# Performance work log

Hardware: AMD Instinct MI355X
Metric: run time of the kernel (lower is better)

## Reference

```python
import jax, jax.numpy as jnp
import numpy as np
import math

B, S, D = 16, 1, 4096
H, KVH, HD = 32, 8, 128
MAXB, MAXS = 16, 4096
R = H // KVH  # n_rep


def _rope(t, cos, sin):
    # t: [B, S, h, HD]; cos/sin: [S, HD//2]
    tf = t.astype(jnp.float32).reshape(*t.shape[:-1], HD // 2, 2)
    a, b = tf[..., 0], tf[..., 1]
    c = cos[None, :, None, :]
    s = sin[None, :, None, :]
    out = jnp.stack([a * c - b * s, a * s + b * c], axis=-1)
    return out.reshape(t.shape).astype(t.dtype)


def setup_inputs() -> dict:
    key = jax.random.key(0)
    ks = jax.random.split(key, 9)
    scale = 1.0 / math.sqrt(D)
    ang = jax.random.uniform(ks[7], (S, HD // 2), jnp.float32) * (2.0 * np.pi)
    return {
        "x": jax.random.normal(ks[0], (B, S, D), jnp.float32),
        "start_pos": 4095,
        "freqs_cos": jnp.cos(ang),
        "freqs_sin": jnp.sin(ang),
        "cache_k": jax.random.normal(ks[1], (MAXB, MAXS, KVH, HD), jnp.float32),
        "cache_v": jax.random.normal(ks[2], (MAXB, MAXS, KVH, HD), jnp.float32),
        "wq": jax.random.normal(ks[3], (D, H * HD), jnp.float32) * scale,
        "wk": jax.random.normal(ks[4], (D, KVH * HD), jnp.float32) * scale,
        "wv": jax.random.normal(ks[5], (D, KVH * HD), jnp.float32) * scale,
        "wo": jax.random.normal(ks[6], (H * HD, D), jnp.float32) * scale,
    }


def reference(x, start_pos, freqs_cos, freqs_sin, cache_k, cache_v, wq, wk, wv, wo):
    bsz, seqlen, _ = x.shape
    xq = (x @ wq).reshape(bsz, seqlen, H, HD)
    xk = (x @ wk).reshape(bsz, seqlen, KVH, HD)
    xv = (x @ wv).reshape(bsz, seqlen, KVH, HD)
    # rotary embeddings on q and k
    xq = _rope(xq, freqs_cos, freqs_sin)
    xk = _rope(xk, freqs_cos, freqs_sin)
    # KV-cache write (start_pos is a static Python int)
    cache_k = cache_k.at[:bsz, start_pos:start_pos + seqlen].set(xk)
    cache_v = cache_v.at[:bsz, start_pos:start_pos + seqlen].set(xv)
    T = start_pos + seqlen
    keys = cache_k[:bsz, :T]    # [B, T, KVH, HD]
    values = cache_v[:bsz, :T]  # [B, T, KVH, HD]
    # GQA: group q heads as [KVH, R] instead of materializing repeated K/V
    q = xq.reshape(bsz, seqlen, KVH, R, HD)
    scores = jnp.einsum("bsgrd,btgd->bgrst", q, keys) / math.sqrt(HD)
    probs = jax.nn.softmax(scores.astype(jnp.float32), axis=-1).astype(xq.dtype)
    out = jnp.einsum("bgrst,btgd->bsgrd", probs, values)
    out = out.reshape(bsz, seqlen, H * HD)
    return out @ wo
```

## Files before the change

### kernel.cpp

```cpp
#include <hip/hip_runtime.h>
#include <hip/hip_bf16.h>
#include <math.h>

#define B 16
#define D 4096
#define H 32
#define KVH 8
#define HD 128
#define R 4
#define T 4096
#define NQKV 6144
#define NCH_A 32
#define NCH_E 32
#define CT 256
#define NCHUNK 16

#define OFF_QKV   0
#define SZ_QKV    (B*NQKV)
#define OFF_ATTN  (OFF_QKV + SZ_QKV)
#define SZ_ATTN   (B*H*HD)
#define OFF_MLO   (OFF_ATTN + SZ_ATTN)
#define SZ_MLO    (B*KVH*NCHUNK*520)
#define OFF_PART  (OFF_ATTN + SZ_ATTN)

__global__ __launch_bounds__(256) void gemv_qkv(
    const float* __restrict__ x, const float* __restrict__ wq,
    const float* __restrict__ wk, const float* __restrict__ wv,
    float* __restrict__ part) {
  int cb = blockIdx.x;
  int ch = blockIdx.y;
  int d0 = ch * 128;
  __shared__ float xT[128][20];
  for (int i = threadIdx.x; i < 128*B; i += 256) {
    int b = i >> 7;
    int d = i & 127;
    xT[d][b] = x[b*D + d0 + d];
  }
  __syncthreads();
  const float* W; int ncols, colbase, outbase;
  if (cb < 16)      { W = wq; ncols = 4096; colbase = cb*256;      outbase = colbase; }
  else if (cb < 20) { W = wk; ncols = 1024; colbase = (cb-16)*256; outbase = 4096 + colbase; }
  else              { W = wv; ncols = 1024; colbase = (cb-20)*256; outbase = 5120 + colbase; }
  int j = colbase + threadIdx.x;
  const float* wp = W + (size_t)d0*ncols + j;
  float acc[16];
  #pragma unroll
  for (int b = 0; b < 16; ++b) acc[b] = 0.f;
  for (int dd = 0; dd < 128; dd += 8) {
    float w[8];
    #pragma unroll
    for (int u = 0; u < 8; ++u) w[u] = wp[(size_t)u*ncols];
    wp += (size_t)8*ncols;
    #pragma unroll
    for (int u = 0; u < 8; ++u) {
      int d = dd + u;
      #pragma unroll
      for (int bq = 0; bq < 4; ++bq) {
        float4 xb = *(const float4*)&xT[d][bq*4];
        acc[bq*4+0] += w[u]*xb.x;
        acc[bq*4+1] += w[u]*xb.y;
        acc[bq*4+2] += w[u]*xb.z;
        acc[bq*4+3] += w[u]*xb.w;
      }
    }
  }
  int outcol = outbase + threadIdx.x;
  #pragma unroll
  for (int b = 0; b < 16; ++b) {
    part[(size_t)ch*SZ_QKV + b*NQKV + outcol] = acc[b];
  }
}

__global__ __launch_bounds__(256) void reduce_rope(
    const float* __restrict__ part, float* __restrict__ qkv,
    const float* __restrict__ fc, const float* __restrict__ fs) {
  int i = blockIdx.x*256 + threadIdx.x;
  int flat = i*2;
  float2 s = make_float2(0.f, 0.f);
  for (int c = 0; c < NCH_A; ++c) {
    float2 v = *(const float2*)&part[(size_t)c*SZ_QKV + flat];
    s.x += v.x; s.y += v.y;
  }
  int col = flat % NQKV;
  if (col < 5120) {
    int jj = (col & 127) >> 1;
    float c = fc[jj], sn = fs[jj];
    float ox = s.x*c - s.y*sn;
    float oy = s.x*sn + s.y*c;
    if (col < 4096) { ox *= 0.08838834764831845f; oy *= 0.08838834764831845f; }
    s.x = ox; s.y = oy;
  }
  *(float2*)&qkv[flat] = s;
}

__global__ __launch_bounds__(256) void attn_kernel(
    const float* __restrict__ qkv, const float* __restrict__ cache_k,
    const float* __restrict__ cache_v, float* __restrict__ mlo) {
  int chunk = blockIdx.x, g = blockIdx.y, b = blockIdx.z;
  int tid = threadIdx.x, wave = tid >> 6, lane = tid & 63;
  __shared__ float q_lds[4][HD];
  __shared__ float4 s_lds4[CT];
  __shared__ float o_lds[4][4][HD];
  for (int i = tid; i < 4*HD; i += 256) {
    int r = i >> 7, d = i & 127;
    q_lds[r][d] = qkv[b*NQKV + (g*R + r)*HD + d];
  }
  __syncthreads();

  int row = wave*64 + lane;
  int tA = chunk*CT + row;
  const float* kp = (tA == T-1) ? &qkv[b*NQKV + 4096 + g*HD]
                    : &cache_k[(((size_t)b*T + tA)*KVH + g)*HD];
  float sA[4] = {0.f,0.f,0.f,0.f};
  #pragma unroll
  for (int bt = 0; bt < 4; ++bt) {
    float4 kreg[8];
    #pragma unroll
    for (int i = 0; i < 8; ++i) kreg[i] = ((const float4*)kp)[bt*8 + i];
    #pragma unroll
    for (int i = 0; i < 8; ++i) {
      int st = bt*8 + i;
      #pragma unroll
      for (int h = 0; h < 4; ++h) {
        float4 qv = *(const float4*)&q_lds[h][st*4];
        sA[h] += kreg[i].x*qv.x + kreg[i].y*qv.y + kreg[i].z*qv.z + kreg[i].w*qv.w;
      }
    }
  }
  s_lds4[row] = make_float4(sA[0], sA[1], sA[2], sA[3]);
  __syncthreads();

  {
    int h = wave;
    float v[4]; float m = -1e30f;
    #pragma unroll
    for (int i = 0; i < 4; ++i) {
      v[i] = ((const float*)&s_lds4[lane + i*64])[h];
      m = fmaxf(m, v[i]);
    }
    for (int off = 32; off > 0; off >>= 1) m = fmaxf(m, __shfl_xor(m, off));
    float l = 0.f;
    #pragma unroll
    for (int i = 0; i < 4; ++i) {
      float p = __expf(v[i] - m);
      ((float*)&s_lds4[lane + i*64])[h] = p;
      l += p;
    }
    for (int off = 32; off > 0; off >>= 1) l += __shfl_xor(l, off);
    if (lane == 0) {
      size_t base = ((size_t)(b*KVH + g)*NCHUNK + chunk)*520;
      mlo[base + h] = m;
      mlo[base + 4 + h] = l;
    }
  }
  __syncthreads();

  int d0 = lane*2;
  float2 acc[4];
  #pragma unroll
  for (int h = 0; h < 4; ++h) acc[h] = make_float2(0.f, 0.f);
  int rbase = wave*64;
  #pragma unroll
  for (int bt = 0; bt < 8; ++bt) {
    float2 vreg[8];
    #pragma unroll
    for (int i = 0; i < 8; ++i) {
      int tl = rbase + bt*8 + i;
      int t = chunk*CT + tl;
      const float* vrow = (t == T-1) ? &qkv[b*NQKV + 5120 + g*HD]
                         : &cache_v[(((size_t)b*T + t)*KVH + g)*HD];
      vreg[i] = *(const float2*)&vrow[d0];
    }
    #pragma unroll
    for (int i = 0; i < 8; ++i) {
      int tl = rbase + bt*8 + i;
      float4 p = s_lds4[tl];
      acc[0].x += p.x*vreg[i].x; acc[0].y += p.x*vreg[i].y;
      acc[1].x += p.y*vreg[i].x; acc[1].y += p.y*vreg[i].y;
      acc[2].x += p.z*vreg[i].x; acc[2].y += p.z*vreg[i].y;
      acc[3].x += p.w*vreg[i].x; acc[3].y += p.w*vreg[i].y;
    }
  }
  #pragma unroll
  for (int h = 0; h < 4; ++h) {
    o_lds[wave][h][d0]   = acc[h].x;
    o_lds[wave][h][d0+1] = acc[h].y;
  }
  __syncthreads();
  size_t base = ((size_t)(b*KVH + g)*NCHUNK + chunk)*520;
  for (int oi = tid; oi < 512; oi += 256) {
    int h = oi >> 7, d = oi & 127;
    float s = 0.f;
    #pragma unroll
    for (int w = 0; w < 4; ++w) s += o_lds[w][h][d];
    mlo[base + 8 + oi] = s;
  }
}

__global__ __launch_bounds__(128) void combine_kernel(
    const float* __restrict__ mlo, float* __restrict__ attn) {
  int g = blockIdx.x, b = blockIdx.y;
  int d = threadIdx.x;
  #pragma unroll
  for (int h = 0; h < 4; ++h) {
    float mc[NCHUNK], lc[NCHUNK];
    float mg = -1e30f;
    #pragma unroll
    for (int c = 0; c < NCHUNK; ++c) {
      size_t base = ((size_t)(b*KVH + g)*NCHUNK + c)*520;
      mc[c] = mlo[base + h];
      lc[c] = mlo[base + 4 + h];
      mg = fmaxf(mg, mc[c]);
    }
    float lg = 0.f, o = 0.f;
    #pragma unroll
    for (int c = 0; c < NCHUNK; ++c) {
      size_t base = ((size_t)(b*KVH + g)*NCHUNK + c)*520;
      float f = __expf(mc[c] - mg);
      lg += f*lc[c];
      o  += f*mlo[base + 8 + h*HD + d];
    }
    attn[b*D + (g*R + h)*HD + d] = o / lg;
  }
}

__global__ __launch_bounds__(256) void gemv_out(
    const float* __restrict__ attn, const float* __restrict__ wo,
    float* __restrict__ part) {
  int cb = blockIdx.x;
  int ch = blockIdx.y;
  int d0 = ch * 128;
  __shared__ float xT[128][20];
  for (int i = threadIdx.x; i < 128*B; i += 256) {
    int b = i >> 7;
    int d = i & 127;
    xT[d][b] = attn[b*D + d0 + d];
  }
  __syncthreads();
  int j = cb*256 + threadIdx.x;
  const float* wp = wo + (size_t)d0*D + j;
  float acc[16];
  #pragma unroll
  for (int b = 0; b < 16; ++b) acc[b] = 0.f;
  for (int dd = 0; dd < 128; dd += 8) {
    float w[8];
    #pragma unroll
    for (int u = 0; u < 8; ++u) w[u] = wp[(size_t)u*D];
    wp += (size_t)8*D;
    #pragma unroll
    for (int u = 0; u < 8; ++u) {
      int d = dd + u;
      #pragma unroll
      for (int bq = 0; bq < 4; ++bq) {
        float4 xb = *(const float4*)&xT[d][bq*4];
        acc[bq*4+0] += w[u]*xb.x;
        acc[bq*4+1] += w[u]*xb.y;
        acc[bq*4+2] += w[u]*xb.z;
        acc[bq*4+3] += w[u]*xb.w;
      }
    }
  }
  #pragma unroll
  for (int b = 0; b < 16; ++b) {
    part[(size_t)ch*SZ_ATTN + b*D + j] = acc[b];
  }
}

__global__ __launch_bounds__(256) void reduce_part(
    const float* __restrict__ part, float* __restrict__ out, int n, int nch) {
  int i = (blockIdx.x*256 + threadIdx.x)*4;
  if (i >= n) return;
  float4 s = make_float4(0.f,0.f,0.f,0.f);
  for (int c = 0; c < nch; ++c) {
    float4 v = *(const float4*)&part[(size_t)c*n + i];
    s.x += v.x; s.y += v.y; s.z += v.z; s.w += v.w;
  }
  *(float4*)&out[i] = s;
}

extern "C" void kernel_launch(void* const* d_in, const int* in_sizes, int n_in,
                              void* d_out, int out_size, void* d_ws, size_t ws_size,
                              hipStream_t stream) {
  const float* x  = (const float*)d_in[0];
  const float* fc = (const float*)d_in[2];
  const float* fs = (const float*)d_in[3];
  const float* ck = (const float*)d_in[4];
  const float* cv = (const float*)d_in[5];
  const float* wq = (const float*)d_in[6];
  const float* wk = (const float*)d_in[7];
  const float* wv = (const float*)d_in[8];
  const float* wo = (const float*)d_in[9];
  float* out  = (float*)d_out;
  float* ws   = (float*)d_ws;
  float* qkv  = ws + OFF_QKV;
  float* attn = ws + OFF_ATTN;
  float* mlo  = ws + OFF_MLO;
  float* part = ws + OFF_PART;

  gemv_qkv<<<dim3(24, NCH_A), 256, 0, stream>>>(x, wq, wk, wv, part);
  reduce_rope<<<dim3(SZ_QKV/512), 256, 0, stream>>>(part, qkv, fc, fs);
  attn_kernel<<<dim3(NCHUNK, KVH, B), 256, 0, stream>>>(qkv, ck, cv, mlo);
  combine_kernel<<<dim3(KVH, B), 128, 0, stream>>>(mlo, attn);
  gemv_out<<<dim3(16, NCH_E), 256, 0, stream>>>(attn, wo, part);
  reduce_part<<<dim3(SZ_ATTN/1024), 256, 0, stream>>>(part, out, SZ_ATTN, NCH_E);
}
```

Before: 201.7 us.

## Restructure attention to process all KV heads per block with LDS-staged K/V tiles

The attention kernel now assigns one block per (batch, 128-token chunk) covering all 8 KV groups and 32 query heads, instead of one block per (chunk, group, batch). Full 4 KB K and V rows are staged into swizzled, double-buffered LDS tiles so global reads are contiguous across all heads. Register-prefetch pipelining overlaps the next row's load with compute. The combine kernel is reorganized per query head over 32 chunks. The aim is better coalescing of cache reads. In exchange, the grid shrinks to 512 blocks, each doing more serial work with a sync per step, and each K row is processed by one wave at a time.

```diff
diff --git a/kernel.cpp b/kernel.cpp
--- a/kernel.cpp
+++ b/kernel.cpp
@@ -12,15 +12,16 @@
 #define NQKV 6144
 #define NCH_A 32
 #define NCH_E 32
-#define CT 256
-#define NCHUNK 16
+#define CT 128
+#define NCHUNK 32
+#define MLOREC 4160
 
 #define OFF_QKV   0
 #define SZ_QKV    (B*NQKV)
 #define OFF_ATTN  (OFF_QKV + SZ_QKV)
 #define SZ_ATTN   (B*H*HD)
 #define OFF_MLO   (OFF_ATTN + SZ_ATTN)
-#define SZ_MLO    (B*KVH*NCHUNK*520)
+#define SZ_MLO    (B*NCHUNK*MLOREC)
 #define OFF_PART  (OFF_ATTN + SZ_ATTN)
 
 __global__ __launch_bounds__(256) void gemv_qkv(
@@ -96,132 +97,166 @@
 __global__ __launch_bounds__(256) void attn_kernel(
     const float* __restrict__ qkv, const float* __restrict__ cache_k,
     const float* __restrict__ cache_v, float* __restrict__ mlo) {
-  int chunk = blockIdx.x, g = blockIdx.y, b = blockIdx.z;
+  int chunk = blockIdx.x, b = blockIdx.y;
   int tid = threadIdx.x, wave = tid >> 6, lane = tid & 63;
-  __shared__ float q_lds[4][HD];
-  __shared__ float4 s_lds4[CT];
-  __shared__ float o_lds[4][4][HD];
-  for (int i = tid; i < 4*HD; i += 256) {
-    int r = i >> 7, d = i & 127;
-    q_lds[r][d] = qkv[b*NQKV + (g*R + r)*HD + d];
+  int t0 = chunk * CT;
+
+  __shared__ float ktile[8][1028];
+  __shared__ float score[CT][33];
+
+  int h = lane & 31, jh = lane >> 5;
+  int g = h >> 2;
+  float4 qreg[16];
+  {
+    const float* qp = qkv + b*NQKV + h*HD + jh*64;
+    #pragma unroll
+    for (int i = 0; i < 16; ++i) qreg[i] = *(const float4*)(qp + i*4);
+  }
+
+  {
+    const float* kbase = cache_k + (size_t)b*T*1024;
+    const float* knew  = qkv + b*NQKV + 4096;
+    {
+      int t = t0 + wave*32;
+      const float* src = (t == T-1) ? knew : (kbase + (size_t)t*1024);
+      float* dst = &ktile[wave*2][0];
+      #pragma unroll
+      for (int it = 0; it < 4; ++it) {
+        float4 v = *(const float4*)(src + (it*64 + lane)*4);
+        int f4 = it*64 + lane;
+        int phys = (f4 & ~31) | ((f4 & 31) ^ ((f4 >> 5) & 7));
+        *(float4*)(dst + phys*4) = v;
+      }
+    }
+    float4 kst[4];
+    for (int p = 0; p < 32; ++p) {
+      if (p+1 < 32) {
+        int t = t0 + wave*32 + p + 1;
+        const float* src = (t == T-1) ? knew : (kbase + (size_t)t*1024);
+        #pragma unroll
+        for (int it = 0; it < 4; ++it)
+          kst[it] = *(const float4*)(src + (it*64 + lane)*4);
+      }
+      const float* krow = &ktile[wave*2 + (p & 1)][0];
+      float s = 0.f;
+      #pragma unroll
+      for (int i = 0; i < 16; ++i) {
+        int phys = g*32 + 16*jh + (i ^ g);
+        float4 kf = *(const float4*)(krow + phys*4);
+        s += kf.x*qreg[i].x + kf.y*qreg[i].y + kf.z*qreg[i].z + kf.w*qreg[i].w;
+      }
+      s += __shfl_xor(s, 32);
+      if (jh == 0) score[wave*32 + p][h] = s;
+      if (p+1 < 32) {
+        float* dst = &ktile[wave*2 + ((p+1) & 1)][0];
+        #pragma unroll
+        for (int it = 0; it < 4; ++it) {
+          int f4 = it*64 + lane;
+          int phys = (f4 & ~31) | ((f4 & 31) ^ ((f4 >> 5) & 7));
+          *(float4*)(dst + phys*4) = kst[it];
+        }
+      }
+    }
   }
   __syncthreads();
 
-  int row = wave*64 + lane;
-  int tA = chunk*CT + row;
-  const float* kp = (tA == T-1) ? &qkv[b*NQKV + 4096 + g*HD]
-                    : &cache_k[(((size_t)b*T + tA)*KVH + g)*HD];
-  float sA[4] = {0.f,0.f,0.f,0.f};
-  #pragma unroll
-  for (int bt = 0; bt < 4; ++bt) {
-    float4 kreg[8];
-    #pragma unroll
-    for (int i = 0; i < 8; ++i) kreg[i] = ((const float4*)kp)[bt*8 + i];
-    #pragma unroll
-    for (int i = 0; i < 8; ++i) {
-      int st = bt*8 + i;
-      #pragma unroll
-      for (int h = 0; h < 4; ++h) {
-        float4 qv = *(const float4*)&q_lds[h][st*4];
-        sA[h] += kreg[i].x*qv.x + kreg[i].y*qv.y + kreg[i].z*qv.z + kreg[i].w*qv.w;
-      }
-    }
-  }
-  s_lds4[row] = make_float4(sA[0], sA[1], sA[2], sA[3]);
+  size_t mbase = ((size_t)b*NCHUNK + chunk)*MLOREC;
+
+  {
+    int hh = tid >> 3, rg = tid & 7;
+    float vv[16]; float m = -1e30f;
+    #pragma unroll
+    for (int i = 0; i < 16; ++i) { vv[i] = score[rg + i*8][hh]; m = fmaxf(m, vv[i]); }
+    m = fmaxf(m, __shfl_xor(m, 1));
+    m = fmaxf(m, __shfl_xor(m, 2));
+    m = fmaxf(m, __shfl_xor(m, 4));
+    float l = 0.f;
+    #pragma unroll
+    for (int i = 0; i < 16; ++i) { float p = __expf(vv[i] - m); score[rg + i*8][hh] = p; l += p; }
+    l += __shfl_xor(l, 1); l += __shfl_xor(l, 2); l += __shfl_xor(l, 4);
+    if (rg == 0) { mlo[mbase + hh] = m; mlo[mbase + 32 + hh] = l; }
+  }
   __syncthreads();
 
   {
-    int h = wave;
-    float v[4]; float m = -1e30f;
-    #pragma unroll
-    for (int i = 0; i < 4; ++i) {
-      v[i] = ((const float*)&s_lds4[lane + i*64])[h];
-      m = fmaxf(m, v[i]);
-    }
-    for (int off = 32; off > 0; off >>= 1) m = fmaxf(m, __shfl_xor(m, off));
-    float l = 0.f;
-    #pragma unroll
-    for (int i = 0; i < 4; ++i) {
-      float p = __expf(v[i] - m);
-      ((float*)&s_lds4[lane + i*64])[h] = p;
-      l += p;
-    }
-    for (int off = 32; off > 0; off >>= 1) l += __shfl_xor(l, off);
-    if (lane == 0) {
-      size_t base = ((size_t)(b*KVH + g)*NCHUNK + chunk)*520;
-      mlo[base + h] = m;
-      mlo[base + 4 + h] = l;
-    }
-  }
-  __syncthreads();
-
-  int d0 = lane*2;
-  float2 acc[4];
-  #pragma unroll
-  for (int h = 0; h < 4; ++h) acc[h] = make_float2(0.f, 0.f);
-  int rbase = wave*64;
-  #pragma unroll
-  for (int bt = 0; bt < 8; ++bt) {
-    float2 vreg[8];
-    #pragma unroll
-    for (int i = 0; i < 8; ++i) {
-      int tl = rbase + bt*8 + i;
-      int t = chunk*CT + tl;
-      const float* vrow = (t == T-1) ? &qkv[b*NQKV + 5120 + g*HD]
-                         : &cache_v[(((size_t)b*T + t)*KVH + g)*HD];
-      vreg[i] = *(const float2*)&vrow[d0];
-    }
-    #pragma unroll
-    for (int i = 0; i < 8; ++i) {
-      int tl = rbase + bt*8 + i;
-      float4 p = s_lds4[tl];
-      acc[0].x += p.x*vreg[i].x; acc[0].y += p.x*vreg[i].y;
-      acc[1].x += p.y*vreg[i].x; acc[1].y += p.y*vreg[i].y;
-      acc[2].x += p.z*vreg[i].x; acc[2].y += p.z*vreg[i].y;
-      acc[3].x += p.w*vreg[i].x; acc[3].y += p.w*vreg[i].y;
-    }
-  }
-  #pragma unroll
-  for (int h = 0; h < 4; ++h) {
-    o_lds[wave][h][d0]   = acc[h].x;
-    o_lds[wave][h][d0+1] = acc[h].y;
-  }
-  __syncthreads();
-  size_t base = ((size_t)(b*KVH + g)*NCHUNK + chunk)*520;
-  for (int oi = tid; oi < 512; oi += 256) {
-    int h = oi >> 7, d = oi & 127;
-    float s = 0.f;
-    #pragma unroll
-    for (int w = 0; w < 4; ++w) s += o_lds[w][h][d];
-    mlo[base + 8 + oi] = s;
+    float* vt = &ktile[0][0];
+    int hv = tid & 31, grp = tid >> 5;
+    int gv = hv >> 2;
+    const float* vbase = cache_v + (size_t)b*T*1024;
+    const float* vnew  = qkv + b*NQKV + 5120;
+    float4 acc0 = make_float4(0.f,0.f,0.f,0.f), acc1 = acc0, acc2 = acc0, acc3 = acc0;
+    int physw = (tid & ~31) | ((tid & 31) ^ ((tid >> 5) & 7));
+    float4 st[4];
+    #pragma unroll
+    for (int ii = 0; ii < 4; ++ii) {
+      int t = t0 + ii;
+      const float* src = (t == T-1) ? vnew : (vbase + (size_t)t*1024);
+      st[ii] = *(const float4*)(src + tid*4);
+    }
+    #pragma unroll
+    for (int ii = 0; ii < 4; ++ii)
+      *(float4*)(vt + ii*1028 + physw*4) = st[ii];
+    __syncthreads();
+    for (int tt = 0; tt < 32; ++tt) {
+      if (tt+1 < 32) {
+        #pragma unroll
+        for (int ii = 0; ii < 4; ++ii) {
+          int t = t0 + (tt+1)*4 + ii;
+          const float* src = (t == T-1) ? vnew : (vbase + (size_t)t*1024);
+          st[ii] = *(const float4*)(src + tid*4);
+        }
+      }
+      const float* buf = vt + (tt & 1)*4*1028;
+      #pragma unroll
+      for (int ii = 0; ii < 4; ++ii) {
+        int row = tt*4 + ii;
+        float p = score[row][hv];
+        const float* vrow = buf + ii*1028;
+        int pb = gv*32;
+        float4 vf0 = *(const float4*)(vrow + (pb + ((grp*4+0) ^ gv))*4);
+        float4 vf1 = *(const float4*)(vrow + (pb + ((grp*4+1) ^ gv))*4);
+        float4 vf2 = *(const float4*)(vrow + (pb + ((grp*4+2) ^ gv))*4);
+        float4 vf3 = *(const float4*)(vrow + (pb + ((grp*4+3) ^ gv))*4);
+        acc0.x += p*vf0.x; acc0.y += p*vf0.y; acc0.z += p*vf0.z; acc0.w += p*vf0.w;
+        acc1.x += p*vf1.x; acc1.y += p*vf1.y; acc1.z += p*vf1.z; acc1.w += p*vf1.w;
+        acc2.x += p*vf2.x; acc2.y += p*vf2.y; acc2.z += p*vf2.z; acc2.w += p*vf2.w;
+        acc3.x += p*vf3.x; acc3.y += p*vf3.y; acc3.z += p*vf3.z; acc3.w += p*vf3.w;
+      }
+      if (tt+1 < 32) {
+        float* dst = vt + ((tt+1) & 1)*4*1028;
+        #pragma unroll
+        for (int ii = 0; ii < 4; ++ii)
+          *(float4*)(dst + ii*1028 + physw*4) = st[ii];
+      }
+      __syncthreads();
+    }
+    float* ob = &mlo[mbase + 64 + (size_t)hv*HD + grp*16];
+    *(float4*)(ob + 0)  = acc0;
+    *(float4*)(ob + 4)  = acc1;
+    *(float4*)(ob + 8)  = acc2;
+    *(float4*)(ob + 12) = acc3;
   }
 }
 
 __global__ __launch_bounds__(128) void combine_kernel(
     const float* __restrict__ mlo, float* __restrict__ attn) {
-  int g = blockIdx.x, b = blockIdx.y;
+  int hh = blockIdx.x;
+  int b = blockIdx.y;
   int d = threadIdx.x;
-  #pragma unroll
-  for (int h = 0; h < 4; ++h) {
-    float mc[NCHUNK], lc[NCHUNK];
-    float mg = -1e30f;
-    #pragma unroll
-    for (int c = 0; c < NCHUNK; ++c) {
-      size_t base = ((size_t)(b*KVH + g)*NCHUNK + c)*520;
-      mc[c] = mlo[base + h];
-      lc[c] = mlo[base + 4 + h];
-      mg = fmaxf(mg, mc[c]);
-    }
-    float lg = 0.f, o = 0.f;
-    #pragma unroll
-    for (int c = 0; c < NCHUNK; ++c) {
-      size_t base = ((size_t)(b*KVH + g)*NCHUNK + c)*520;
-      float f = __expf(mc[c] - mg);
-      lg += f*lc[c];
-      o  += f*mlo[base + 8 + h*HD + d];
-    }
-    attn[b*D + (g*R + h)*HD + d] = o / lg;
-  }
+  size_t base0 = (size_t)b*NCHUNK*MLOREC;
+  float mg = -1e30f;
+  #pragma unroll 8
+  for (int c = 0; c < NCHUNK; ++c)
+    mg = fmaxf(mg, mlo[base0 + (size_t)c*MLOREC + hh]);
+  float lg = 0.f, o = 0.f;
+  #pragma unroll 4
+  for (int c = 0; c < NCHUNK; ++c) {
+    size_t bb = base0 + (size_t)c*MLOREC;
+    float f = __expf(mlo[bb + hh] - mg);
+    lg += f*mlo[bb + 32 + hh];
+    o  += f*mlo[bb + 64 + hh*HD + d];
+  }
+  attn[b*D + hh*HD + d] = o / lg;
 }
 
 __global__ __launch_bounds__(256) void gemv_out(
@@ -299,8 +334,8 @@
 
   gemv_qkv<<<dim3(24, NCH_A), 256, 0, stream>>>(x, wq, wk, wv, part);
   reduce_rope<<<dim3(SZ_QKV/512), 256, 0, stream>>>(part, qkv, fc, fs);
-  attn_kernel<<<dim3(NCHUNK, KVH, B), 256, 0, stream>>>(qkv, ck, cv, mlo);
-  combine_kernel<<<dim3(KVH, B), 128, 0, stream>>>(mlo, attn);
+  attn_kernel<<<dim3(NCHUNK, B), 256, 0, stream>>>(qkv, ck, cv, mlo);
+  combine_kernel<<<dim3(H, B), 128, 0, stream>>>(mlo, attn);
   gemv_out<<<dim3(16, NCH_E), 256, 0, stream>>>(attn, wo, part);
   reduce_part<<<dim3(SZ_ATTN/1024), 256, 0, stream>>>(part, out, SZ_ATTN, NCH_E);
 }
```

Result: faster. 187.0 us (-7.3%).
